# Kernel optimization log

Hardware: AMD Instinct MI355X
Metric: run time of the kernel (lower is better)

The kernel has to match this reference:

```python
import jax, jax.numpy as jnp
import numpy as np

B, N, D, H = 8, 2048, 128, 128  # batch, num_nodes, input_size, hidden_size


def setup_inputs() -> dict:
    key = jax.random.key(0)
    ks = jax.random.split(key, 10)
    s = 1.0 / np.sqrt(H)
    u = lambda k, shape: jax.random.uniform(k, shape, jnp.float32, -s, s)
    return {
        "x": jax.random.normal(ks[0], (B, N, D), jnp.float32),
        "adj_matrix": jax.random.randint(ks[1], (B, N, N), 0, 2, jnp.int32),
        # PyTorch LSTM params, gate order (i, f, g, o); forward + backward dirs
        "w_ih_f": u(ks[2], (4 * H, D)),
        "w_hh_f": u(ks[3], (4 * H, H)),
        "b_ih_f": u(ks[4], (4 * H,)),
        "b_hh_f": u(ks[5], (4 * H,)),
        "w_ih_b": u(ks[6], (4 * H, D)),
        "w_hh_b": u(ks[7], (4 * H, H)),
        "b_ih_b": u(ks[8], (4 * H,)),
        "b_hh_b": u(ks[9], (4 * H,)),
    }


def _lstm_last_h(xp, w_hh):
    # xp: [T, B, 4H] precomputed input projection + biases; returns final h [B, H]
    b = xp.shape[1]
    h0 = jnp.zeros((b, H), xp.dtype)
    c0 = jnp.zeros((b, H), xp.dtype)

    def step(carry, xt):
        h, c = carry
        gates = xt + h @ w_hh.T
        i, f, g, o = jnp.split(gates, 4, axis=-1)
        c = jax.nn.sigmoid(f) * c + jax.nn.sigmoid(i) * jnp.tanh(g)
        h = jax.nn.sigmoid(o) * jnp.tanh(c)
        return (h, c), None

    (hT, _), _ = jax.lax.scan(step, (h0, c0), xp)
    return hT


def reference(x, adj_matrix, w_ih_f, w_hh_f, b_ih_f, b_hh_f, w_ih_b, w_hh_b, b_ih_b, b_hh_b):
    x = x.astype(jnp.float32)
    a = (adj_matrix > 0).astype(jnp.float32)  # [B, N, N]
    # mean over {self} + neighbors: (x_i + sum_j a_ij x_j) / (1 + deg_i)
    deg = a.sum(-1, keepdims=True)
    xa = (x + jnp.einsum('bij,bjd->bid', a, x)) / (1.0 + deg)  # [B, N, D]

    seq = jnp.swapaxes(xa, 0, 1)  # [N, B, D], time-major over nodes
    hT_f = _lstm_last_h(seq @ w_ih_f.T + (b_ih_f + b_hh_f), w_hh_f)
    hT_b = _lstm_last_h(seq[::-1] @ w_ih_b.T + (b_ih_b + b_hh_b), w_hh_b)
    return jnp.concatenate([hT_f, hT_b], axis=-1)  # [B, 2H]
```

## Files before the change

### kernel.cpp

```cpp
#include <hip/hip_runtime.h>
#include <math.h>

#define BB 8
#define NN 2048
#define DD 128
#define HH 128

typedef float f4 __attribute__((ext_vector_type(4)));

__device__ __forceinline__ float fast_rcp(float x) { return __builtin_amdgcn_rcpf(x); }

#define TI 32
#define TJ 64

__global__ __launch_bounds__(256) void k_agg(const float* __restrict__ x,
                                             const int* __restrict__ adj,
                                             float* __restrict__ xa) {
    __shared__ __align__(16) float xs[TJ][132];
    __shared__ __align__(16) float as[TI][68];
    const int b = blockIdx.y;
    const int i0 = blockIdx.x * TI;
    const int tid = threadIdx.x;
    const int ig = tid >> 5;
    const int dg = tid & 31;
    const float* xb = x + (size_t)b * NN * DD;
    const int* ab = adj + (size_t)b * NN * NN;

    float acc[4][4];
    float deg[4];
#pragma unroll
    for (int i = 0; i < 4; ++i) {
        deg[i] = 0.f;
#pragma unroll
        for (int d = 0; d < 4; ++d) acc[i][d] = 0.f;
    }

    for (int j0 = 0; j0 < NN; j0 += TJ) {
#pragma unroll
        for (int k = 0; k < 8; ++k) {
            int idx = tid + k * 256;
            int row = idx >> 5, c4 = idx & 31;
            float4 v = *(const float4*)(xb + (size_t)(j0 + row) * DD + c4 * 4);
            *(float4*)(&xs[row][c4 * 4]) = v;
        }
#pragma unroll
        for (int k = 0; k < 2; ++k) {
            int idx = tid + k * 256;
            int row = idx >> 4, c4 = idx & 15;
            int4 v = *(const int4*)(ab + (size_t)(i0 + row) * NN + j0 + c4 * 4);
            float4 f;
            f.x = v.x > 0 ? 1.f : 0.f;
            f.y = v.y > 0 ? 1.f : 0.f;
            f.z = v.z > 0 ? 1.f : 0.f;
            f.w = v.w > 0 ? 1.f : 0.f;
            *(float4*)(&as[row][c4 * 4]) = f;
        }
        __syncthreads();
#pragma unroll 4
        for (int jq = 0; jq < TJ; jq += 4) {
            float4 av[4], xv[4];
#pragma unroll
            for (int i = 0; i < 4; ++i) av[i] = *(const float4*)(&as[ig * 4 + i][jq]);
#pragma unroll
            for (int jj = 0; jj < 4; ++jj) xv[jj] = *(const float4*)(&xs[jq + jj][dg * 4]);
#pragma unroll
            for (int i = 0; i < 4; ++i) {
                const float* ap = (const float*)&av[i];
#pragma unroll
                for (int jj = 0; jj < 4; ++jj) {
                    float a = ap[jj];
                    const float* xp4 = (const float*)&xv[jj];
                    deg[i] += a;
                    acc[i][0] = fmaf(a, xp4[0], acc[i][0]);
                    acc[i][1] = fmaf(a, xp4[1], acc[i][1]);
                    acc[i][2] = fmaf(a, xp4[2], acc[i][2]);
                    acc[i][3] = fmaf(a, xp4[3], acc[i][3]);
                }
            }
        }
        __syncthreads();
    }
#pragma unroll
    for (int i = 0; i < 4; ++i) {
        int gi = i0 + ig * 4 + i;
        float r = fast_rcp(1.f + deg[i]);
        float4 xv = *(const float4*)(xb + (size_t)gi * DD + dg * 4);
        float4 o;
        o.x = (xv.x + acc[i][0]) * r;
        o.y = (xv.y + acc[i][1]) * r;
        o.z = (xv.z + acc[i][2]) * r;
        o.w = (xv.w + acc[i][3]) * r;
        *(float4*)(xa + ((size_t)b * NN + gi) * DD + dg * 4) = o;
    }
}

#define MT 64
#define GT 32

__global__ __launch_bounds__(256) void k_proj(const float* __restrict__ xa,
                                              const float* __restrict__ wif,
                                              const float* __restrict__ wib,
                                              const float* __restrict__ bif,
                                              const float* __restrict__ bhf,
                                              const float* __restrict__ bib,
                                              const float* __restrict__ bhb,
                                              float* __restrict__ xpf,
                                              float* __restrict__ xpb) {
    __shared__ __align__(16) float xs[MT][132];
    __shared__ __align__(16) float wl[GT][132];
    const int r0 = blockIdx.x * MT;
    const int g0 = blockIdx.y * GT;
    const int tid = threadIdx.x;
#pragma unroll
    for (int k = 0; k < 8; ++k) {
        int idx = tid + k * 256;
        int row = idx >> 5, c4 = idx & 31;
        int r = r0 + row;
        int t = r >> 3, bb = r & 7;
        float4 v = *(const float4*)(xa + ((size_t)bb * NN + t) * DD + c4 * 4);
        *(float4*)(&xs[row][c4 * 4]) = v;
    }
#pragma unroll
    for (int k = 0; k < 4; ++k) {
        int idx = tid + k * 256;
        int row = idx >> 5, c4 = idx & 31;
        int g = g0 + row;
        const float* wsrc = (g < 512) ? (wif + (size_t)g * DD) : (wib + (size_t)(g - 512) * DD);
        *(float4*)(&wl[row][c4 * 4]) = *(const float4*)(wsrc + c4 * 4);
    }
    __syncthreads();
    const int mg = tid >> 4;
    const int gg = tid & 15;
    float acc[4][2];
#pragma unroll
    for (int i = 0; i < 4; ++i) { acc[i][0] = 0.f; acc[i][1] = 0.f; }
#pragma unroll 8
    for (int d4 = 0; d4 < 32; ++d4) {
        float4 xv[4], wv[2];
#pragma unroll
        for (int i = 0; i < 4; ++i) xv[i] = *(const float4*)(&xs[mg * 4 + i][d4 * 4]);
        wv[0] = *(const float4*)(&wl[gg * 2 + 0][d4 * 4]);
        wv[1] = *(const float4*)(&wl[gg * 2 + 1][d4 * 4]);
#pragma unroll
        for (int i = 0; i < 4; ++i) {
#pragma unroll
            for (int j = 0; j < 2; ++j) {
                acc[i][j] = fmaf(xv[i].x, wv[j].x, acc[i][j]);
                acc[i][j] = fmaf(xv[i].y, wv[j].y, acc[i][j]);
                acc[i][j] = fmaf(xv[i].z, wv[j].z, acc[i][j]);
                acc[i][j] = fmaf(xv[i].w, wv[j].w, acc[i][j]);
            }
        }
    }
#pragma unroll
    for (int j = 0; j < 2; ++j) {
        int g = g0 + gg * 2 + j;
        float bias = (g < 512) ? (bif[g] + bhf[g]) : (bib[g - 512] + bhb[g - 512]);
#pragma unroll
        for (int i = 0; i < 4; ++i) {
            int r = r0 + mg * 4 + i;
            int t = r >> 3, bb = r & 7;
            float v = acc[i][j] + bias;
            if (g < 512) {
                int p = 4 * (g & 127) + (g >> 7);
                xpf[((size_t)t * BB + bb) * 512 + p] = v;
            } else {
                int gb = g - 512;
                int p = 4 * (gb & 127) + (gb >> 7);
                xpb[((size_t)(NN - 1 - t) * BB + bb) * 512 + p] = v;
            }
        }
    }
}


#define STRG(x) #x
#define WLD(R0, R3, WOFF, IMM)                                            \
    "global_load_dwordx4 v[" STRG(R0) ":" STRG(R3) "], %[" STRG(WOFF) "], %[whs] offset:" STRG(IMM) "\n\t"
#define PKQ(H0, H1, A0, A1, B0, B1, C0, C1, D0, D1)                                        \
    "v_pk_fma_f32 v[24:25], v[" STRG(A0) ":" STRG(A1) "], v[" STRG(H0) ":" STRG(H1) "], v[24:25]\n\t" \
    "v_pk_fma_f32 v[26:27], v[" STRG(B0) ":" STRG(B1) "], v[" STRG(H0) ":" STRG(H1) "], v[26:27]\n\t" \
    "v_pk_fma_f32 v[28:29], v[" STRG(C0) ":" STRG(C1) "], v[" STRG(H0) ":" STRG(H1) "], v[28:29]\n\t" \
    "v_pk_fma_f32 v[30:31], v[" STRG(D0) ":" STRG(D1) "], v[" STRG(H0) ":" STRG(H1) "], v[30:31]\n\t"

__global__ __launch_bounds__(512) void k_lstm(const float* __restrict__ xpf,
                                              const float* __restrict__ xpb,
                                              const float* __restrict__ whf,
                                              const float* __restrict__ whb,
                                              float* __restrict__ out) {
    const int b = blockIdx.x;
    const int dir = blockIdx.y;
    const float* __restrict__ xp = dir ? xpb : xpf;
    const float* __restrict__ wh = dir ? whb : whf;
    const int t = threadIdx.x;
    const int q = t >> 2;
    const int jq = t & 3;

    __shared__ __align__(64) float h_lds[1088];
    for (int i = t; i < 1088; i += 512) h_lds[i] = 0.f;
    __syncthreads();

    unsigned hbase = (unsigned)(uintptr_t)&h_lds[0];
    unsigned rd0 = hbase + 672u * (unsigned)jq;
    unsigned rdd = rd0 ^ (rd0 + 2176u);
    unsigned wr0 = hbase + 2176u + 544u * (unsigned)jq + ((unsigned)q << 2);
    unsigned wrd = wr0 ^ (wr0 - 2176u);
    unsigned w0 = ((0u * 128u + (unsigned)q) * 128u + (unsigned)jq * 32u) * 4u;
    unsigned w1 = ((1u * 128u + (unsigned)q) * 128u + (unsigned)jq * 32u) * 4u;
    unsigned w2 = ((2u * 128u + (unsigned)q) * 128u + (unsigned)jq * 32u) * 4u;
    unsigned w3 = ((3u * 128u + (unsigned)q) * 128u + (unsigned)jq * 32u) * 4u;
    unsigned xoff = (unsigned)(b * 512 + t) * 4u + 16384u;
    float xp0v = xp[(size_t)b * 512 + t];
    float sel0 = (jq == 0) ? 1.f : 0.f;
    float sel1 = (jq == 1) ? 1.f : 0.f;
    float sel2 = (jq == 2) ? 1.f : 0.f;
    float sel3 = (jq == 3) ? 1.f : 0.f;
    float h_out;

    asm volatile(
        "v_mov_b32 v16, 0\n\t"
        "v_mov_b32 v18, 0x800\n\t"
        "v_mov_b32 v19, %[x0]\n\t"
        "v_mov_b32 v21, %[xo]\n\t"
        "v_mov_b32 v22, %[rdb]\n\t"
        "v_mov_b32 v23, %[wrb]\n\t"
        WLD(64, 67, w0, 0) WLD(68, 71, w0, 16) WLD(72, 75, w0, 32) WLD(76, 79, w0, 48)
        WLD(80, 83, w0, 64) WLD(84, 87, w0, 80) WLD(88, 91, w0, 96) WLD(92, 95, w0, 112)
        WLD(96, 99, w1, 0) WLD(100, 103, w1, 16) WLD(104, 107, w1, 32) WLD(108, 111, w1, 48)
        WLD(112, 115, w1, 64) WLD(116, 119, w1, 80) WLD(120, 123, w1, 96) WLD(124, 127, w1, 112)
        WLD(128, 131, w2, 0) WLD(132, 135, w2, 16) WLD(136, 139, w2, 32) WLD(140, 143, w2, 48)
        WLD(144, 147, w2, 64) WLD(148, 151, w2, 80) WLD(152, 155, w2, 96) WLD(156, 159, w2, 112)
        WLD(160, 163, w3, 0) WLD(164, 167, w3, 16) WLD(168, 171, w3, 32) WLD(172, 175, w3, 48)
        WLD(176, 179, w3, 64) WLD(180, 183, w3, 80) WLD(184, 187, w3, 96) WLD(188, 191, w3, 112)
        "s_waitcnt vmcnt(0)\n\t"
        "LSTM_TOP%=:\n\t"
        "global_load_dword v20, v21, %[xps]\n\t"
        "ds_read_b128 v[32:35], v22\n\t"
        "ds_read_b128 v[36:39], v22 offset:16\n\t"
        "ds_read_b128 v[40:43], v22 offset:32\n\t"
        "ds_read_b128 v[44:47], v22 offset:48\n\t"
        "ds_read_b128 v[48:51], v22 offset:64\n\t"
        "ds_read_b128 v[52:55], v22 offset:80\n\t"
        "ds_read_b128 v[56:59], v22 offset:96\n\t"
        "ds_read_b128 v[60:63], v22 offset:112\n\t"
        "v_mul_f32 v24, %[s0], v19\n\t"
        "v_mov_b32 v25, 0\n\t"
        "v_mul_f32 v26, %[s1], v19\n\t"
        "v_mov_b32 v27, 0\n\t"
        "v_mul_f32 v28, %[s2], v19\n\t"
        "v_mov_b32 v29, 0\n\t"
        "v_mul_f32 v30, %[s3], v19\n\t"
        "v_mov_b32 v31, 0\n\t"
        "s_waitcnt lgkmcnt(0)\n\t"
        PKQ(32, 33, 64, 65, 96, 97, 128, 129, 160, 161)
        PKQ(34, 35, 66, 67, 98, 99, 130, 131, 162, 163)
        PKQ(36, 37, 68, 69, 100, 101, 132, 133, 164, 165)
        PKQ(38, 39, 70, 71, 102, 103, 134, 135, 166, 167)
        PKQ(40, 41, 72, 73, 104, 105, 136, 137, 168, 169)
        PKQ(42, 43, 74, 75, 106, 107, 138, 139, 170, 171)
        PKQ(44, 45, 76, 77, 108, 109, 140, 141, 172, 173)
        PKQ(46, 47, 78, 79, 110, 111, 142, 143, 174, 175)
        PKQ(48, 49, 80, 81, 112, 113, 144, 145, 176, 177)
        PKQ(50, 51, 82, 83, 114, 115, 146, 147, 178, 179)
        PKQ(52, 53, 84, 85, 116, 117, 148, 149, 180, 181)
        PKQ(54, 55, 86, 87, 118, 119, 150, 151, 182, 183)
        PKQ(56, 57, 88, 89, 120, 121, 152, 153, 184, 185)
        PKQ(58, 59, 90, 91, 122, 123, 154, 155, 186, 187)
        PKQ(60, 61, 92, 93, 124, 125, 156, 157, 188, 189)
        PKQ(62, 63, 94, 95, 126, 127, 158, 159, 190, 191)
        "v_add_f32 v8, v24, v25\n\t"
        "v_add_f32 v9, v26, v27\n\t"
        "v_add_f32 v10, v28, v29\n\t"
        "v_add_f32 v11, v30, v31\n\t"
        "v_mov_b32_dpp v12, v8 quad_perm:[1,0,3,2] row_mask:0xf bank_mask:0xf\n\t"
        "v_mov_b32_dpp v13, v9 quad_perm:[1,0,3,2] row_mask:0xf bank_mask:0xf\n\t"
        "v_mov_b32_dpp v14, v10 quad_perm:[1,0,3,2] row_mask:0xf bank_mask:0xf\n\t"
        "v_mov_b32_dpp v15, v11 quad_perm:[1,0,3,2] row_mask:0xf bank_mask:0xf\n\t"
        "v_add_f32 v8, v8, v12\n\t"
        "v_add_f32 v9, v9, v13\n\t"
        "v_add_f32 v10, v10, v14\n\t"
        "v_add_f32 v11, v11, v15\n\t"
        "v_mov_b32_dpp v12, v8 quad_perm:[2,3,0,1] row_mask:0xf bank_mask:0xf\n\t"
        "v_mov_b32_dpp v13, v9 quad_perm:[2,3,0,1] row_mask:0xf bank_mask:0xf\n\t"
        "v_mov_b32_dpp v14, v10 quad_perm:[2,3,0,1] row_mask:0xf bank_mask:0xf\n\t"
        "v_mov_b32_dpp v15, v11 quad_perm:[2,3,0,1] row_mask:0xf bank_mask:0xf\n\t"
        "v_add_f32 v8, v8, v12\n\t"
        "v_add_f32 v9, v9, v13\n\t"
        "v_add_f32 v10, v10, v14\n\t"
        "v_add_f32 v11, v11, v15\n\t"
        "v_mul_f32 v12, 0xbfb8aa3b, v8\n\t"
        "v_mul_f32 v13, 0xbfb8aa3b, v9\n\t"
        "v_mul_f32 v14, 0xc038aa3b, v10\n\t"
        "v_mul_f32 v15, 0xbfb8aa3b, v11\n\t"
        "v_exp_f32 v12, v12\n\t"
        "v_exp_f32 v13, v13\n\t"
        "v_exp_f32 v14, v14\n\t"
        "v_exp_f32 v15, v15\n\t"
        "v_add_f32 v12, 1.0, v12\n\t"
        "v_add_f32 v13, 1.0, v13\n\t"
        "v_add_f32 v14, 1.0, v14\n\t"
        "v_add_f32 v15, 1.0, v15\n\t"
        "v_rcp_f32 v12, v12\n\t"
        "v_rcp_f32 v13, v13\n\t"
        "v_rcp_f32 v14, v14\n\t"
        "v_rcp_f32 v15, v15\n\t"
        "s_nop 0\n\t"
        "v_fma_f32 v14, 2.0, v14, -1.0\n\t"
        "v_mul_f32 v12, v12, v14\n\t"
        "v_fma_f32 v16, v13, v16, v12\n\t"
        "v_mul_f32 v14, 0xc038aa3b, v16\n\t"
        "v_exp_f32 v14, v14\n\t"
        "s_nop 1\n\t"
        "v_add_f32 v14, 1.0, v14\n\t"
        "v_rcp_f32 v14, v14\n\t"
        "s_nop 1\n\t"
        "v_fma_f32 v14, 2.0, v14, -1.0\n\t"
        "v_mul_f32 v17, v14, v15\n\t"
        "ds_write_b32 v23, v17\n\t"
        "s_waitcnt vmcnt(0) lgkmcnt(0)\n\t"
        "v_mov_b32 v19, v20\n\t"
        "s_barrier\n\t"
        "v_add_u32 v18, -1, v18\n\t"
        "v_cmp_ne_u32 vcc, 0, v18\n\t"
        "v_xor_b32 v22, %[rdd], v22\n\t"
        "v_xor_b32 v23, %[wrd], v23\n\t"
        "v_add_u32 v21, 0x4000, v21\n\t"
        "s_cbranch_vccnz LSTM_TOP%=\n\t"
        "v_mov_b32 %[ho], v17\n\t"
        : [ho] "=v"(h_out)
        : [w0] "v"(w0), [w1] "v"(w1), [w2] "v"(w2), [w3] "v"(w3),
          [whs] "s"(wh), [xps] "s"(xp),
          [xo] "v"(xoff), [rdb] "v"(rd0), [wrb] "v"(wr0),
          [rdd] "v"(rdd), [wrd] "v"(wrd), [x0] "v"(xp0v),
          [s0] "v"(sel0), [s1] "v"(sel1), [s2] "v"(sel2), [s3] "v"(sel3)
        : "memory", "vcc",
          "v8", "v9", "v10", "v11", "v12", "v13", "v14", "v15", "v16", "v17",
          "v18", "v19", "v20", "v21", "v22", "v23", "v24", "v25", "v26", "v27",
          "v28", "v29", "v30", "v31", "v32", "v33", "v34", "v35", "v36", "v37",
          "v38", "v39", "v40", "v41", "v42", "v43", "v44", "v45", "v46", "v47",
          "v48", "v49", "v50", "v51", "v52", "v53", "v54", "v55", "v56", "v57",
          "v58", "v59", "v60", "v61", "v62", "v63", "v64", "v65", "v66", "v67",
          "v68", "v69", "v70", "v71", "v72", "v73", "v74", "v75", "v76", "v77",
          "v78", "v79", "v80", "v81", "v82", "v83", "v84", "v85", "v86", "v87",
          "v88", "v89", "v90", "v91", "v92", "v93", "v94", "v95", "v96", "v97",
          "v98", "v99", "v100", "v101", "v102", "v103", "v104", "v105", "v106", "v107",
          "v108", "v109", "v110", "v111", "v112", "v113", "v114", "v115", "v116", "v117",
          "v118", "v119", "v120", "v121", "v122", "v123", "v124", "v125", "v126", "v127",
          "v128", "v129", "v130", "v131", "v132", "v133", "v134", "v135", "v136", "v137",
          "v138", "v139", "v140", "v141", "v142", "v143", "v144", "v145", "v146", "v147",
          "v148", "v149", "v150", "v151", "v152", "v153", "v154", "v155", "v156", "v157",
          "v158", "v159", "v160", "v161", "v162", "v163", "v164", "v165", "v166", "v167",
          "v168", "v169", "v170", "v171", "v172", "v173", "v174", "v175", "v176", "v177",
          "v178", "v179", "v180", "v181", "v182", "v183", "v184", "v185", "v186", "v187",
          "v188", "v189", "v190", "v191");

    if (jq == 0) out[(size_t)b * 256 + dir * HH + q] = h_out;
}

extern "C" void kernel_launch(void* const* d_in, const int* in_sizes, int n_in,
                              void* d_out, int out_size, void* d_ws, size_t ws_size,
                              hipStream_t stream) {
    const float* x = (const float*)d_in[0];
    const int* adj = (const int*)d_in[1];
    const float* wif = (const float*)d_in[2];
    const float* whf = (const float*)d_in[3];
    const float* bif = (const float*)d_in[4];
    const float* bhf = (const float*)d_in[5];
    const float* wib = (const float*)d_in[6];
    const float* whb = (const float*)d_in[7];
    const float* bib = (const float*)d_in[8];
    const float* bhb = (const float*)d_in[9];
    float* out = (float*)d_out;

    float* xpf = (float*)d_ws;
    float* xpb = xpf + (size_t)NN * BB * 512;
    float* xa = xpb + (size_t)NN * BB * 512;

    k_agg<<<dim3(NN / TI, BB), 256, 0, stream>>>(x, adj, xa);
    k_proj<<<dim3((NN * BB) / MT, 1024 / GT), 256, 0, stream>>>(xa, wif, wib, bif, bhf, bib, bhb,
                                                                xpf, xpb);
    k_lstm<<<dim3(BB, 2), 512, 0, stream>>>(xpf, xpb, whf, whb, out);
}
```

Baseline: 1.469 ms.

## Overlap LDS reads with FMAs, distribute gate activations across quad lanes

Replaces the single lgkmcnt(0) wait with staggered waits, so packed FMAs start as each ds_read_b128 arrives. The first FMA becomes a pk_mul, which drops the accumulator initialisation. The x projection is now added after the reduction, and each lane in a quad computes only its own gate's activation using per-lane constants, then broadcasts via DPP instead of computing all four. The loop counter moves to a scalar register with a scalar branch. This adds DPP broadcasts and a few nops to the serial step in exchange for fewer transcendental ops and less LDS latency on the critical path.

```diff
diff --git a/kernel.cpp b/kernel.cpp
--- a/kernel.cpp
+++ b/kernel.cpp
@@ -182,6 +182,11 @@
     "v_pk_fma_f32 v[26:27], v[" STRG(B0) ":" STRG(B1) "], v[" STRG(H0) ":" STRG(H1) "], v[26:27]\n\t" \
     "v_pk_fma_f32 v[28:29], v[" STRG(C0) ":" STRG(C1) "], v[" STRG(H0) ":" STRG(H1) "], v[28:29]\n\t" \
     "v_pk_fma_f32 v[30:31], v[" STRG(D0) ":" STRG(D1) "], v[" STRG(H0) ":" STRG(H1) "], v[30:31]\n\t"
+#define PKQ0(H0, H1, A0, A1, B0, B1, C0, C1, D0, D1)                                       \
+    "v_pk_mul_f32 v[24:25], v[" STRG(A0) ":" STRG(A1) "], v[" STRG(H0) ":" STRG(H1) "]\n\t" \
+    "v_pk_mul_f32 v[26:27], v[" STRG(B0) ":" STRG(B1) "], v[" STRG(H0) ":" STRG(H1) "]\n\t" \
+    "v_pk_mul_f32 v[28:29], v[" STRG(C0) ":" STRG(C1) "], v[" STRG(H0) ":" STRG(H1) "]\n\t" \
+    "v_pk_mul_f32 v[30:31], v[" STRG(D0) ":" STRG(D1) "], v[" STRG(H0) ":" STRG(H1) "]\n\t"
 
 __global__ __launch_bounds__(512) void k_lstm(const float* __restrict__ xpf,
                                               const float* __restrict__ xpb,
@@ -211,15 +216,18 @@
     unsigned w3 = ((3u * 128u + (unsigned)q) * 128u + (unsigned)jq * 32u) * 4u;
     unsigned xoff = (unsigned)(b * 512 + t) * 4u + 16384u;
     float xp0v = xp[(size_t)b * 512 + t];
-    float sel0 = (jq == 0) ? 1.f : 0.f;
-    float sel1 = (jq == 1) ? 1.f : 0.f;
-    float sel2 = (jq == 2) ? 1.f : 0.f;
-    float sel3 = (jq == 3) ? 1.f : 0.f;
+    float s0 = (jq == 0) ? 1.f : 0.f;
+    float s1 = (jq == 1) ? 1.f : 0.f;
+    float s2 = (jq == 2) ? 1.f : 0.f;
+    float s3 = (jq == 3) ? 1.f : 0.f;
+    float mlv = (jq == 2) ? -2.8853900817779268f : -1.4426950408889634f;
+    float Aav = (jq == 2) ? 2.f : 1.f;
+    float Bav = (jq == 2) ? -1.f : 0.f;
     float h_out;
 
     asm volatile(
         "v_mov_b32 v16, 0\n\t"
-        "v_mov_b32 v18, 0x800\n\t"
+        "s_movk_i32 s20, 0x800\n\t"
         "v_mov_b32 v19, %[x0]\n\t"
         "v_mov_b32 v21, %[xo]\n\t"
         "v_mov_b32 v22, %[rdb]\n\t"
@@ -243,29 +251,30 @@
         "ds_read_b128 v[52:55], v22 offset:80\n\t"
         "ds_read_b128 v[56:59], v22 offset:96\n\t"
         "ds_read_b128 v[60:63], v22 offset:112\n\t"
-        "v_mul_f32 v24, %[s0], v19\n\t"
-        "v_mov_b32 v25, 0\n\t"
-        "v_mul_f32 v26, %[s1], v19\n\t"
-        "v_mov_b32 v27, 0\n\t"
-        "v_mul_f32 v28, %[s2], v19\n\t"
-        "v_mov_b32 v29, 0\n\t"
-        "v_mul_f32 v30, %[s3], v19\n\t"
-        "v_mov_b32 v31, 0\n\t"
-        "s_waitcnt lgkmcnt(0)\n\t"
-        PKQ(32, 33, 64, 65, 96, 97, 128, 129, 160, 161)
+        "v_xor_b32 v22, %[rdd], v22\n\t"
+        "v_add_u32 v21, 0x4000, v21\n\t"
+        "s_waitcnt lgkmcnt(7)\n\t"
+        PKQ0(32, 33, 64, 65, 96, 97, 128, 129, 160, 161)
         PKQ(34, 35, 66, 67, 98, 99, 130, 131, 162, 163)
+        "s_waitcnt lgkmcnt(6)\n\t"
         PKQ(36, 37, 68, 69, 100, 101, 132, 133, 164, 165)
         PKQ(38, 39, 70, 71, 102, 103, 134, 135, 166, 167)
+        "s_waitcnt lgkmcnt(5)\n\t"
         PKQ(40, 41, 72, 73, 104, 105, 136, 137, 168, 169)
         PKQ(42, 43, 74, 75, 106, 107, 138, 139, 170, 171)
+        "s_waitcnt lgkmcnt(4)\n\t"
         PKQ(44, 45, 76, 77, 108, 109, 140, 141, 172, 173)
         PKQ(46, 47, 78, 79, 110, 111, 142, 143, 174, 175)
+        "s_waitcnt lgkmcnt(3)\n\t"
         PKQ(48, 49, 80, 81, 112, 113, 144, 145, 176, 177)
         PKQ(50, 51, 82, 83, 114, 115, 146, 147, 178, 179)
+        "s_waitcnt lgkmcnt(2)\n\t"
         PKQ(52, 53, 84, 85, 116, 117, 148, 149, 180, 181)
         PKQ(54, 55, 86, 87, 118, 119, 150, 151, 182, 183)
+        "s_waitcnt lgkmcnt(1)\n\t"
         PKQ(56, 57, 88, 89, 120, 121, 152, 153, 184, 185)
         PKQ(58, 59, 90, 91, 122, 123, 154, 155, 186, 187)
+        "s_waitcnt lgkmcnt(0)\n\t"
         PKQ(60, 61, 92, 93, 124, 125, 156, 157, 188, 189)
         PKQ(62, 63, 94, 95, 126, 127, 158, 159, 190, 191)
         "v_add_f32 v8, v24, v25\n\t"
@@ -288,26 +297,25 @@
         "v_add_f32 v9, v9, v13\n\t"
         "v_add_f32 v10, v10, v14\n\t"
         "v_add_f32 v11, v11, v15\n\t"
-        "v_mul_f32 v12, 0xbfb8aa3b, v8\n\t"
-        "v_mul_f32 v13, 0xbfb8aa3b, v9\n\t"
-        "v_mul_f32 v14, 0xc038aa3b, v10\n\t"
-        "v_mul_f32 v15, 0xbfb8aa3b, v11\n\t"
-        "v_exp_f32 v12, v12\n\t"
+        "v_mul_f32 v12, %[s0], v8\n\t"
+        "v_fma_f32 v12, %[s1], v9, v12\n\t"
+        "v_fma_f32 v12, %[s2], v10, v12\n\t"
+        "v_fma_f32 v12, %[s3], v11, v12\n\t"
+        "v_add_f32 v12, v12, v19\n\t"
+        "v_mul_f32 v13, %[ml], v12\n\t"
         "v_exp_f32 v13, v13\n\t"
-        "v_exp_f32 v14, v14\n\t"
-        "v_exp_f32 v15, v15\n\t"
-        "v_add_f32 v12, 1.0, v12\n\t"
+        "s_nop 1\n\t"
         "v_add_f32 v13, 1.0, v13\n\t"
-        "v_add_f32 v14, 1.0, v14\n\t"
-        "v_add_f32 v15, 1.0, v15\n\t"
-        "v_rcp_f32 v12, v12\n\t"
         "v_rcp_f32 v13, v13\n\t"
-        "v_rcp_f32 v14, v14\n\t"
-        "v_rcp_f32 v15, v15\n\t"
-        "s_nop 0\n\t"
-        "v_fma_f32 v14, 2.0, v14, -1.0\n\t"
-        "v_mul_f32 v12, v12, v14\n\t"
-        "v_fma_f32 v16, v13, v16, v12\n\t"
+        "s_nop 1\n\t"
+        "v_fma_f32 v12, %[Aa], v13, %[Ba]\n\t"
+        "s_nop 1\n\t"
+        "v_mov_b32_dpp v13, v12 quad_perm:[0,0,0,0] row_mask:0xf bank_mask:0xf\n\t"
+        "v_mov_b32_dpp v14, v12 quad_perm:[2,2,2,2] row_mask:0xf bank_mask:0xf\n\t"
+        "v_mov_b32_dpp v15, v12 quad_perm:[1,1,1,1] row_mask:0xf bank_mask:0xf\n\t"
+        "v_mov_b32_dpp v17, v12 quad_perm:[3,3,3,3] row_mask:0xf bank_mask:0xf\n\t"
+        "v_mul_f32 v13, v13, v14\n\t"
+        "v_fma_f32 v16, v15, v16, v13\n\t"
         "v_mul_f32 v14, 0xc038aa3b, v16\n\t"
         "v_exp_f32 v14, v14\n\t"
         "s_nop 1\n\t"
@@ -315,25 +323,24 @@
         "v_rcp_f32 v14, v14\n\t"
         "s_nop 1\n\t"
         "v_fma_f32 v14, 2.0, v14, -1.0\n\t"
-        "v_mul_f32 v17, v14, v15\n\t"
+        "v_mul_f32 v17, v14, v17\n\t"
         "ds_write_b32 v23, v17\n\t"
         "s_waitcnt vmcnt(0) lgkmcnt(0)\n\t"
         "v_mov_b32 v19, v20\n\t"
         "s_barrier\n\t"
-        "v_add_u32 v18, -1, v18\n\t"
-        "v_cmp_ne_u32 vcc, 0, v18\n\t"
-        "v_xor_b32 v22, %[rdd], v22\n\t"
         "v_xor_b32 v23, %[wrd], v23\n\t"
-        "v_add_u32 v21, 0x4000, v21\n\t"
-        "s_cbranch_vccnz LSTM_TOP%=\n\t"
+        "s_sub_u32 s20, s20, 1\n\t"
+        "s_cmp_lg_u32 s20, 0\n\t"
+        "s_cbranch_scc1 LSTM_TOP%=\n\t"
         "v_mov_b32 %[ho], v17\n\t"
         : [ho] "=v"(h_out)
         : [w0] "v"(w0), [w1] "v"(w1), [w2] "v"(w2), [w3] "v"(w3),
           [whs] "s"(wh), [xps] "s"(xp),
           [xo] "v"(xoff), [rdb] "v"(rd0), [wrb] "v"(wr0),
           [rdd] "v"(rdd), [wrd] "v"(wrd), [x0] "v"(xp0v),
-          [s0] "v"(sel0), [s1] "v"(sel1), [s2] "v"(sel2), [s3] "v"(sel3)
-        : "memory", "vcc",
+          [s0] "v"(s0), [s1] "v"(s1), [s2] "v"(s2), [s3] "v"(s3),
+          [ml] "v"(mlv), [Aa] "v"(Aav), [Ba] "v"(Bav)
+        : "memory", "vcc", "scc", "s20",
           "v8", "v9", "v10", "v11", "v12", "v13", "v14", "v15", "v16", "v17",
           "v18", "v19", "v20", "v21", "v22", "v23", "v24", "v25", "v26", "v27",
           "v28", "v29", "v30", "v31", "v32", "v33", "v34", "v35", "v36", "v37",
```

After: 1.363 ms. 1.08x faster.
